# Kernel optimization log

Hardware: AMD Instinct MI355X
Metric: run time of the kernel (lower is better)

The kernel has to match this reference:

```python
import jax, jax.numpy as jnp
import numpy as np

N_HEAD = 16
D_HEAD = 64


def setup_inputs() -> dict:
    key = jax.random.key(0)
    k1, k2, k3, k4 = jax.random.split(key, 4)
    T, B, D = 1024, 8, 1024
    input = jax.random.normal(k1, (T, B, D), dtype=jnp.float32)
    pos_enc = jax.random.normal(k2, (T, B, D), dtype=jnp.float32) * 0.1
    # causal mask: True = masked (future positions), broadcast over batch
    causal = jnp.triu(jnp.ones((T, T), dtype=bool), k=1)
    attn_mask = jnp.broadcast_to(causal[None, :, :], (B, T, T))
    W_qkv = jax.random.normal(k3, (D, 3 * N_HEAD * D_HEAD), dtype=jnp.float32) * (D ** -0.5)
    W_o = jax.random.normal(k4, (N_HEAD * D_HEAD, N_HEAD * D_HEAD), dtype=jnp.float32) * ((N_HEAD * D_HEAD) ** -0.5)
    return {"input": input, "pos_enc": pos_enc, "attn_mask": attn_mask,
            "W_qkv": W_qkv, "W_o": W_o}


def reference(input, pos_enc, attn_mask, W_qkv, W_o):
    T, B, D = input.shape
    scale = 1.0 / (D_HEAD ** 0.5)
    # attn_type == 2: qkv on (w + r)
    heads = (input + pos_enc) @ W_qkv                      # [T,B,3*n*d]
    q, k, v = jnp.split(heads, 3, axis=-1)
    q = q.reshape(T, B, N_HEAD, D_HEAD)
    k = k.reshape(T, B, N_HEAD, D_HEAD)
    v = v.reshape(T, B, N_HEAD, D_HEAD)
    # scores [B, n, qlen, klen]
    score = jnp.einsum('ibnd,jbnd->bnij', q, k) * scale
    score = jnp.where(attn_mask[:, None, :, :], -jnp.inf, score)
    prob = jax.nn.softmax(score.astype(jnp.float32), axis=-1)  # [B,n,i,j]
    # coverage: mean over heads -> [B,i,j], then transpose -> [B,j,i]
    coverage = jnp.mean(prob, axis=1).transpose(0, 2, 1)
    # dropout is identity at eval (dropatt=0)
    attn_vec = jnp.einsum('bnij,jbnd->ibnd', prob, v)       # [T,B,n,d]
    attn_vec = attn_vec.reshape(T, B, N_HEAD * D_HEAD)
    attn_out = attn_vec @ W_o
    return attn_out, coverage
```

## Files before the change

kernel.cpp:

```cpp
#include <hip/hip_runtime.h>
#include <hip/hip_bf16.h>


typedef __bf16 v8bf __attribute__((ext_vector_type(8)));
typedef float  v4f  __attribute__((ext_vector_type(4)));
typedef unsigned short v8us __attribute__((ext_vector_type(8)));

#define MFMA16x16x32(a, b, c) __builtin_amdgcn_mfma_f32_16x16x32_bf16(a, b, c, 0, 0, 0)

#define GLD_LDS16(g, l) \
    __builtin_amdgcn_global_load_lds((const __attribute__((address_space(1))) void*)(g), \
                                     (__attribute__((address_space(3))) void*)(l), 16, 0, 0)

__device__ __forceinline__ unsigned short f2bf(float f) {
    unsigned int u = __float_as_uint(f);
    u = (u + 0x7FFF + ((u >> 16) & 1)) >> 16;
    return (unsigned short)u;
}

__global__ __launch_bounds__(256) void prep_x(const float* __restrict__ in,
                                              const float* __restrict__ pe,
                                              unsigned short* __restrict__ x) {
    size_t idx = ((size_t)blockIdx.x * 256 + threadIdx.x) * 8;
    v4f a0 = *(const v4f*)(in + idx);
    v4f a1 = *(const v4f*)(in + idx + 4);
    v4f p0 = *(const v4f*)(pe + idx);
    v4f p1 = *(const v4f*)(pe + idx + 4);
    v8us r;
    unsigned short* rp = (unsigned short*)&r;
#pragma unroll
    for (int q = 0; q < 4; q++) {
        rp[q]     = f2bf(a0[q] + p0[q]);
        rp[q + 4] = f2bf(a1[q] + p1[q]);
    }
    *(v8us*)(x + idx) = r;
}

__global__ __launch_bounds__(256) void transpose_f32_bf16(const float* __restrict__ src,
                                                          unsigned short* __restrict__ dst,
                                                          int R, int C) {
    __shared__ alignas(16) unsigned short t[64][72];
    int c0 = blockIdx.x * 64, r0 = blockIdx.y * 64;
    int tid = threadIdx.x;
    int rr = tid >> 2, cg = (tid & 3) * 16;
    const float* s = src + (size_t)(r0 + rr) * C + c0 + cg;
#pragma unroll
    for (int q4 = 0; q4 < 4; q4++) {
        v4f v = *(const v4f*)(s + q4 * 4);
#pragma unroll
        for (int q = 0; q < 4; q++) t[rr][cg + q4 * 4 + q] = f2bf(v[q]);
    }
    __syncthreads();
    v8us o0, o1;
    unsigned short* o0p = (unsigned short*)&o0;
    unsigned short* o1p = (unsigned short*)&o1;
#pragma unroll
    for (int q = 0; q < 8; q++) {
        o0p[q] = t[cg + q][rr];
        o1p[q] = t[cg + 8 + q][rr];
    }
    *(v8us*)(dst + (size_t)(c0 + rr) * R + r0 + cg)     = o0;
    *(v8us*)(dst + (size_t)(c0 + rr) * R + r0 + cg + 8) = o1;
}

__global__ __launch_bounds__(256) void transpose_v(const unsigned short* __restrict__ heads,
                                                   unsigned short* __restrict__ Vt) {
    __shared__ alignas(16) unsigned short t[64][72];
    const int bn = blockIdx.y, b = bn >> 4, n = bn & 15;
    const int j0 = blockIdx.x * 64;
    const int tid = threadIdx.x;
    const int jr = tid >> 2, dg = (tid & 3) * 16;
    const unsigned short* s = heads + ((size_t)(j0 + jr) * 8 + b) * 3072 + 2048 + n * 64 + dg;
    *(v8us*)&t[jr][dg]     = *(const v8us*)(s);
    *(v8us*)&t[jr][dg + 8] = *(const v8us*)(s + 8);
    __syncthreads();
    const int dr = tid >> 2, jg = (tid & 3) * 16;
    v8us o0, o1;
    unsigned short* o0p = (unsigned short*)&o0;
    unsigned short* o1p = (unsigned short*)&o1;
#pragma unroll
    for (int q = 0; q < 8; q++) {
        o0p[q] = t[jg + q][dr];
        o1p[q] = t[jg + 8 + q][dr];
    }
    unsigned short* d = Vt + ((size_t)bn * 64 + dr) * 1024 + j0 + jg;
    *(v8us*)(d)     = o0;
    *(v8us*)(d + 8) = o1;
}

template <bool F32OUT>
__global__ __launch_bounds__(256) void gemm_bf16_v2(const unsigned short* __restrict__ A,
                                                    const unsigned short* __restrict__ Bt,
                                                    void* __restrict__ Cout,
                                                    int M, int N, int K) {
    __shared__ alignas(16) unsigned short As[128 * 64];
    __shared__ alignas(16) unsigned short Bs[128 * 64];

    const int nwgx = gridDim.x;
    const int id   = blockIdx.y * nwgx + blockIdx.x;
    const int cpx  = (nwgx * gridDim.y) >> 3;
    const int id2  = (id & 7) * cpx + (id >> 3);
    const int m0 = (id2 / nwgx) * 128, n0 = (id2 % nwgx) * 128;

    const int tid = threadIdx.x;
    const int lane = tid & 63, wave = tid >> 6;
    const int quad = lane >> 4, lq = lane & 15, lq7 = lq & 7;
    const int mW = (wave & 1) * 64, nW = (wave >> 1) * 64;

    v4f acc[4][4];
#pragma unroll
    for (int mi = 0; mi < 4; mi++)
#pragma unroll
        for (int ni = 0; ni < 4; ni++) acc[mi][ni] = (v4f){0.f, 0.f, 0.f, 0.f};

    const int lr = lane >> 3, lu = lane & 7;
    const int ug = lu ^ lr;
    const unsigned short* agl = A  + (size_t)(m0 + wave * 32 + lr) * K + ug * 8;
    const unsigned short* bgl = Bt + (size_t)(n0 + wave * 32 + lr) * K + ug * 8;
    unsigned short* AsW = (unsigned short*)As + wave * 32 * 64;
    unsigned short* BsW = (unsigned short*)Bs + wave * 32 * 64;

    for (int k0 = 0; k0 < K; k0 += 64) {
        __syncthreads();
#pragma unroll
        for (int t = 0; t < 4; t++) {
            GLD_LDS16(agl + k0 + (size_t)t * 8 * K, AsW + t * 512);
            GLD_LDS16(bgl + k0 + (size_t)t * 8 * K, BsW + t * 512);
        }
        __syncthreads();
#pragma unroll
        for (int h = 0; h < 2; h++) {
            v8bf af[4], bfr[4];
#pragma unroll
            for (int mi = 0; mi < 4; mi++)
                af[mi] = *(const v8bf*)&As[(mW + mi * 16 + lq) * 64 + (((quad + 4 * h) ^ lq7) * 8)];
#pragma unroll
            for (int ni = 0; ni < 4; ni++)
                bfr[ni] = *(const v8bf*)&Bs[(nW + ni * 16 + lq) * 64 + (((quad + 4 * h) ^ lq7) * 8)];
#pragma unroll
            for (int mi = 0; mi < 4; mi++)
#pragma unroll
                for (int ni = 0; ni < 4; ni++)
                    acc[mi][ni] = MFMA16x16x32(af[mi], bfr[ni], acc[mi][ni]);
        }
    }

#pragma unroll
    for (int mi = 0; mi < 4; mi++)
#pragma unroll
        for (int ni = 0; ni < 4; ni++)
#pragma unroll
            for (int r = 0; r < 4; r++) {
                int row = m0 + mW + mi * 16 + quad * 4 + r;
                int col = n0 + nW + ni * 16 + lq;
                if (F32OUT)
                    ((float*)Cout)[(size_t)row * N + col] = acc[mi][ni][r];
                else
                    ((unsigned short*)Cout)[(size_t)row * N + col] = f2bf(acc[mi][ni][r]);
            }
}

#define AT_T  1024
#define AT_B  8
#define AT_NH 16
#define AT_HS 3072
#define AT_ALPHA 0.18033688011112042f

__global__ __launch_bounds__(256) void attn_fused5(const unsigned short* __restrict__ heads,
                                                   const unsigned short* __restrict__ Vt,
                                                   unsigned short* __restrict__ av,
                                                   float* __restrict__ lBuf) {
    __shared__ alignas(16) unsigned short KL[64 * 64];
    __shared__ alignas(16) unsigned short VL[64 * 64];
    __shared__ alignas(16) unsigned short Ps[4 * 16 * 32];
    const int bn = blockIdx.x, b = bn >> 4, n = bn & 15;
    const int y = blockIdx.y;
    const int g = (y < 8) ? (15 - y) : (y - 8);
    const int tid = threadIdx.x;
    const int wv = tid >> 6, lane = tid & 63;
    const int quad = lane >> 4, lq = lane & 15;
    const int i0 = g * 64 + wv * 16;
    const int imax = i0 + 15;

    size_t qbase = ((size_t)(i0 + lq) * 8 + b) * AT_HS + n * 64 + quad * 8;
    v8bf q0 = *(const v8bf*)(heads + qbase);
    v8bf q1 = *(const v8bf*)(heads + qbase + 32);

    const int srow = tid >> 3, sunit = tid & 7;
    const size_t kRowStride = (size_t)8 * AT_HS;
    const unsigned short* kg = heads + ((size_t)srow * 8 + b) * AT_HS + 1024 + n * 64 + sunit * 8;
    const unsigned short* vg = Vt + ((size_t)bn * 64 + srow) * 1024 + sunit * 8;
    const int swz = ((sunit ^ (srow & 7)) * 8);
    unsigned short* kw0 = KL + srow * 64 + swz;
    unsigned short* kw1 = KL + (srow + 32) * 64 + swz;
    unsigned short* vw0 = VL + srow * 64 + swz;
    unsigned short* vw1 = VL + (srow + 32) * 64 + swz;

    v8us kr0 = *(const v8us*)(kg);
    v8us kr1 = *(const v8us*)(kg + 32 * kRowStride);
    v8us vr0 = *(const v8us*)(vg);
    v8us vr1 = *(const v8us*)(vg + 32 * 1024);

    unsigned short* psw = Ps + wv * 512;
    const v8bf* pr = (const v8bf*)(psw + lq * 32 + ((quad ^ (lq & 3)) * 8));
    const int lq7 = lq & 7, lqh = lq >> 3;

    float Sl[4] = {0.f, 0.f, 0.f, 0.f};
    v4f o[4];
#pragma unroll
    for (int dt = 0; dt < 4; dt++) o[dt] = (v4f){0.f, 0.f, 0.f, 0.f};

    for (int c = 0; c <= g; ++c) {
        __syncthreads();
        *(v8us*)kw0 = kr0; *(v8us*)kw1 = kr1;
        *(v8us*)vw0 = vr0; *(v8us*)vw1 = vr1;
        __syncthreads();
        if (c < g) {
            const unsigned short* kgn = kg + (size_t)(c + 1) * 64 * kRowStride;
            kr0 = *(const v8us*)(kgn);
            kr1 = *(const v8us*)(kgn + 32 * kRowStride);
            const unsigned short* vgn = vg + (c + 1) * 64;
            vr0 = *(const v8us*)(vgn);
            vr1 = *(const v8us*)(vgn + 32 * 1024);
        }
        const int jb = c * 64;
#pragma unroll
        for (int jj = 0; jj < 64; jj += 32) {
            const int j0 = jb + jj;
            if (j0 <= imax) {
                const v8bf ka = *(const v8bf*)(KL + (jj + lq) * 64      + ((quad ^ lq7) * 8));
                const v8bf kb = *(const v8bf*)(KL + (jj + lq) * 64      + (((4 + quad) ^ lq7) * 8));
                const v8bf kc = *(const v8bf*)(KL + (jj + 16 + lq) * 64 + ((quad ^ lq7) * 8));
                const v8bf kd = *(const v8bf*)(KL + (jj + 16 + lq) * 64 + (((4 + quad) ^ lq7) * 8));
                v4f s0 = (v4f){0.f, 0.f, 0.f, 0.f}, s1 = s0;
                s0 = MFMA16x16x32(q0, ka, s0);
                s0 = MFMA16x16x32(q1, kb, s0);
                s1 = MFMA16x16x32(q0, kc, s1);
                s1 = MFMA16x16x32(q1, kd, s1);
                const int ja = j0 + lq, jb2 = j0 + 16 + lq;
#pragma unroll
                for (int r = 0; r < 4; ++r) {
                    const int i = i0 + quad * 4 + r;
                    float e0 = exp2f(s0[r] * AT_ALPHA);
                    float e1 = exp2f(s1[r] * AT_ALPHA);
                    float p0 = (ja  <= i) ? e0 : 0.f;
                    float p1 = (jb2 <= i) ? e1 : 0.f;
                    Sl[r] += p0 + p1;
                    psw[(quad * 4 + r) * 32 + ((lqh ^ r) * 8) + lq7]        = f2bf(p0);
                    psw[(quad * 4 + r) * 32 + (((lqh | 2) ^ r) * 8) + lq7]  = f2bf(p1);
                }
                const v8bf pf = *pr;
#pragma unroll
                for (int dt = 0; dt < 4; ++dt) {
                    const v8bf vf = *(const v8bf*)(VL + (dt * 16 + lq) * 64 +
                                                   ((((jj >> 3) + quad) ^ lq7) * 8));
                    o[dt] = MFMA16x16x32(pf, vf, o[dt]);
                }
            }
        }
    }

#pragma unroll
    for (int mask = 1; mask < 16; mask <<= 1)
#pragma unroll
        for (int r = 0; r < 4; r++)
            Sl[r] += __shfl_xor(Sl[r], mask);
    float linv[4];
#pragma unroll
    for (int r = 0; r < 4; r++) linv[r] = __builtin_amdgcn_rcpf(Sl[r]);
    if (lq == 0) {
#pragma unroll
        for (int r = 0; r < 4; r++) {
            int i = i0 + quad * 4 + r;
            lBuf[(size_t)bn * AT_T + i] = Sl[r];
        }
    }
#pragma unroll
    for (int dt = 0; dt < 4; dt++)
#pragma unroll
        for (int r = 0; r < 4; r++) {
            int i = i0 + quad * 4 + r;
            av[((size_t)i * 8 + b) * 1024 + n * 64 + dt * 16 + lq] = f2bf(o[dt][r] * linv[r]);
        }
}

__global__ __launch_bounds__(256) void coverage3(const unsigned short* __restrict__ heads,
                                                 const float* __restrict__ lBuf,
                                                 float* __restrict__ cov) {
    const int jt64 = blockIdx.x, it64 = blockIdx.y, b = blockIdx.z;
    const int i0 = it64 * 64, j0 = jt64 * 64;
    const int tid = threadIdx.x;

    if (jt64 > it64) {
        float* base = cov + (size_t)b * 1048576 + (size_t)(j0 + (tid >> 2)) * 1024
                      + i0 + (tid & 3) * 16;
        v4f z = (v4f){0.f, 0.f, 0.f, 0.f};
#pragma unroll
        for (int q = 0; q < 4; q++) *(v4f*)(base + q * 4) = z;
        return;
    }

    __shared__ alignas(16) char smem[64 * 68 * 4];
    unsigned short* QL = (unsigned short*)smem;
    unsigned short* KL = (unsigned short*)(smem + 8192);
    float* TF = (float*)smem;

    const int wv = tid >> 6, lane = tid & 63;
    const int quad = lane >> 4, lq = lane & 15, lq7 = lq & 7;
    const bool diag = (it64 == jt64);
    const int jtmax = diag ? wv : 3;

    const int srow = tid >> 3, sunit = tid & 7;
    const unsigned short* qgb = heads + ((size_t)(i0 + srow) * 8 + b) * AT_HS + sunit * 8;
    const unsigned short* kgb = heads + ((size_t)(j0 + srow) * 8 + b) * AT_HS + 1024 + sunit * 8;
    const int rowOff32 = 32 * 8 * AT_HS;
    const int swz = (sunit ^ (srow & 7)) * 8;
    unsigned short* qw0 = QL + srow * 64 + swz;
    unsigned short* qw1 = QL + (srow + 32) * 64 + swz;
    unsigned short* kw0 = KL + srow * 64 + swz;
    unsigned short* kw1 = KL + (srow + 32) * 64 + swz;

    v8us qr0 = *(const v8us*)(qgb);
    v8us qr1 = *(const v8us*)(qgb + rowOff32);
    v8us kr0 = *(const v8us*)(kgb);
    v8us kr1 = *(const v8us*)(kgb + rowOff32);

    v4f acc[4];
#pragma unroll
    for (int jt = 0; jt < 4; jt++) acc[jt] = (v4f){0.f, 0.f, 0.f, 0.f};

    const float* lrow = lBuf + (size_t)b * 16 * AT_T + i0 + wv * 16 + quad * 4;

    for (int n = 0; n < 16; ++n) {
        __syncthreads();
        *(v8us*)qw0 = qr0; *(v8us*)qw1 = qr1;
        *(v8us*)kw0 = kr0; *(v8us*)kw1 = kr1;
        __syncthreads();
        if (n < 15) {
            qr0 = *(const v8us*)(qgb + (n + 1) * 64);
            qr1 = *(const v8us*)(qgb + (n + 1) * 64 + rowOff32);
            kr0 = *(const v8us*)(kgb + (n + 1) * 64);
            kr1 = *(const v8us*)(kgb + (n + 1) * 64 + rowOff32);
        }
        v4f lv = *(const v4f*)(lrow + (size_t)n * AT_T);
        float linv[4];
#pragma unroll
        for (int r = 0; r < 4; r++) linv[r] = __builtin_amdgcn_rcpf(lv[r]);

        const v8bf qa = *(const v8bf*)(QL + (wv * 16 + lq) * 64 + ((quad ^ lq7) * 8));
        const v8bf qb = *(const v8bf*)(QL + (wv * 16 + lq) * 64 + (((4 + quad) ^ lq7) * 8));
#pragma unroll
        for (int jt = 0; jt < 4; jt++) {
            if (jt <= jtmax) {
                const v8bf ka = *(const v8bf*)(KL + (jt * 16 + lq) * 64 + ((quad ^ lq7) * 8));
                const v8bf kb = *(const v8bf*)(KL + (jt * 16 + lq) * 64 + (((4 + quad) ^ lq7) * 8));
                v4f s = (v4f){0.f, 0.f, 0.f, 0.f};
                s = MFMA16x16x32(qa, ka, s);
                s = MFMA16x16x32(qb, kb, s);
#pragma unroll
                for (int r = 0; r < 4; r++) {
                    float e = exp2f(s[r] * AT_ALPHA);
                    if (diag && jt == wv && lq > quad * 4 + r) e = 0.f;
                    acc[jt][r] = fmaf(e, linv[r], acc[jt][r]);
                }
            }
        }
    }

    __syncthreads();
#pragma unroll
    for (int jt = 0; jt < 4; jt++) {
        v4f w = acc[jt] * 0.0625f;
        *(v4f*)(TF + (size_t)(jt * 16 + lq) * 68 + wv * 16 + quad * 4) = w;
    }
    __syncthreads();
    {
        const int jl = tid >> 2, cg = (tid & 3) * 16;
        float* dst = cov + (size_t)b * 1048576 + (size_t)(j0 + jl) * 1024 + i0 + cg;
        const float* src = TF + (size_t)jl * 68 + cg;
#pragma unroll
        for (int q = 0; q < 4; q++) *(v4f*)(dst + q * 4) = *(const v4f*)(src + q * 4);
    }
}

extern "C" void kernel_launch(void* const* d_in, const int* in_sizes, int n_in,
                              void* d_out, int out_size, void* d_ws, size_t ws_size,
                              hipStream_t stream) {
    const float* input = (const float*)d_in[0];
    const float* pos   = (const float*)d_in[1];
    const float* Wqkv  = (const float*)d_in[3];
    const float* Wo    = (const float*)d_in[4];
    float* out = (float*)d_out;

    char* ws = (char*)d_ws;
    if (ws_size < 93323264) return;
    unsigned short* x     = (unsigned short*)(ws);
    unsigned short* heads = (unsigned short*)(ws + 16777216);
    unsigned short* av    = (unsigned short*)(ws + 67108864);
    unsigned short* WqkvT = (unsigned short*)(ws + 83886080);
    unsigned short* WoT   = (unsigned short*)(ws + 90177536);
    float* lBuf = (float*)(ws + 92798976);
    unsigned short* Vt = x;

    prep_x<<<4096, 256, 0, stream>>>(input, pos, x);
    transpose_f32_bf16<<<dim3(48, 16), 256, 0, stream>>>(Wqkv, WqkvT, 1024, 3072);
    transpose_f32_bf16<<<dim3(16, 16), 256, 0, stream>>>(Wo, WoT, 1024, 1024);
    gemm_bf16_v2<false><<<dim3(24, 64), 256, 0, stream>>>(x, WqkvT, heads, 8192, 3072, 1024);
    transpose_v<<<dim3(16, 128), 256, 0, stream>>>(heads, Vt);
    attn_fused5<<<dim3(128, 16), 256, 0, stream>>>(heads, Vt, av, lBuf);
    coverage3<<<dim3(16, 16, 8), 256, 0, stream>>>(heads, lBuf, out + 8388608);
    gemm_bf16_v2<true><<<dim3(8, 64), 256, 0, stream>>>(av, WoT, out, 8192, 1024, 1024);
}
```

Measured before the change: 337.8 us.

## Fuse prep kernels and double-buffer K with direct Q loads in coverage

Merges the input-add and the two weight-transpose kernels into one launch, which removes two kernel launches. The coverage kernel now reads Q fragments straight from global memory into registers instead of staging them through LDS. K tiles are double-buffered in LDS, cutting the per-head barriers from two to one. The row-tile order is also reversed so the heavier lower-triangle blocks get scheduled first. The risk is less coalesced Q reads from global memory.

New measurement: 361.1 us. 1.07x slower.

```diff
diff --git a/kernel.cpp b/kernel.cpp
--- a/kernel.cpp
+++ b/kernel.cpp
@@ -18,30 +18,11 @@
     return (unsigned short)u;
 }
 
-__global__ __launch_bounds__(256) void prep_x(const float* __restrict__ in,
-                                              const float* __restrict__ pe,
-                                              unsigned short* __restrict__ x) {
-    size_t idx = ((size_t)blockIdx.x * 256 + threadIdx.x) * 8;
-    v4f a0 = *(const v4f*)(in + idx);
-    v4f a1 = *(const v4f*)(in + idx + 4);
-    v4f p0 = *(const v4f*)(pe + idx);
-    v4f p1 = *(const v4f*)(pe + idx + 4);
-    v8us r;
-    unsigned short* rp = (unsigned short*)&r;
-#pragma unroll
-    for (int q = 0; q < 4; q++) {
-        rp[q]     = f2bf(a0[q] + p0[q]);
-        rp[q + 4] = f2bf(a1[q] + p1[q]);
-    }
-    *(v8us*)(x + idx) = r;
-}
-
-__global__ __launch_bounds__(256) void transpose_f32_bf16(const float* __restrict__ src,
-                                                          unsigned short* __restrict__ dst,
-                                                          int R, int C) {
-    __shared__ alignas(16) unsigned short t[64][72];
-    int c0 = blockIdx.x * 64, r0 = blockIdx.y * 64;
-    int tid = threadIdx.x;
+__device__ __forceinline__ void transpose_tile_f32_bf16(const float* __restrict__ src,
+                                                        unsigned short* __restrict__ dst,
+                                                        int R, int C, int bx, int by,
+                                                        int tid, unsigned short (*t)[72]) {
+    int c0 = bx * 64, r0 = by * 64;
     int rr = tid >> 2, cg = (tid & 3) * 16;
     const float* s = src + (size_t)(r0 + rr) * C + c0 + cg;
 #pragma unroll
@@ -61,6 +42,38 @@
     }
     *(v8us*)(dst + (size_t)(c0 + rr) * R + r0 + cg)     = o0;
     *(v8us*)(dst + (size_t)(c0 + rr) * R + r0 + cg + 8) = o1;
+}
+
+__global__ __launch_bounds__(256) void prep_all(const float* __restrict__ in,
+                                                const float* __restrict__ pe,
+                                                unsigned short* __restrict__ x,
+                                                const float* __restrict__ Wqkv,
+                                                unsigned short* __restrict__ WqkvT,
+                                                const float* __restrict__ Wo,
+                                                unsigned short* __restrict__ WoT) {
+    __shared__ alignas(16) unsigned short t[64][72];
+    const int id = blockIdx.x, tid = threadIdx.x;
+    if (id < 4096) {
+        size_t idx = ((size_t)id * 256 + tid) * 8;
+        v4f a0 = *(const v4f*)(in + idx);
+        v4f a1 = *(const v4f*)(in + idx + 4);
+        v4f p0 = *(const v4f*)(pe + idx);
+        v4f p1 = *(const v4f*)(pe + idx + 4);
+        v8us r;
+        unsigned short* rp = (unsigned short*)&r;
+#pragma unroll
+        for (int q = 0; q < 4; q++) {
+            rp[q]     = f2bf(a0[q] + p0[q]);
+            rp[q + 4] = f2bf(a1[q] + p1[q]);
+        }
+        *(v8us*)(x + idx) = r;
+    } else if (id < 4864) {
+        int r = id - 4096;
+        transpose_tile_f32_bf16(Wqkv, WqkvT, 1024, 3072, r % 48, r / 48, tid, t);
+    } else {
+        int r = id - 4864;
+        transpose_tile_f32_bf16(Wo, WoT, 1024, 1024, r % 16, r / 16, tid, t);
+    }
 }
 
 __global__ __launch_bounds__(256) void transpose_v(const unsigned short* __restrict__ heads,
@@ -284,10 +297,10 @@
         }
 }
 
-__global__ __launch_bounds__(256) void coverage3(const unsigned short* __restrict__ heads,
+__global__ __launch_bounds__(256) void coverage4(const unsigned short* __restrict__ heads,
                                                  const float* __restrict__ lBuf,
                                                  float* __restrict__ cov) {
-    const int jt64 = blockIdx.x, it64 = blockIdx.y, b = blockIdx.z;
+    const int jt64 = blockIdx.x, it64 = 15 - blockIdx.y, b = blockIdx.z;
     const int i0 = it64 * 64, j0 = jt64 * 64;
     const int tid = threadIdx.x;
 
@@ -300,9 +313,9 @@
         return;
     }
 
-    __shared__ alignas(16) char smem[64 * 68 * 4];
-    unsigned short* QL = (unsigned short*)smem;
-    unsigned short* KL = (unsigned short*)(smem + 8192);
+    __shared__ alignas(16) char smem[17408];
+    unsigned short* KL0 = (unsigned short*)smem;
+    unsigned short* KL1 = (unsigned short*)(smem + 8192);
     float* TF = (float*)smem;
 
     const int wv = tid >> 6, lane = tid & 63;
@@ -311,19 +324,13 @@
     const int jtmax = diag ? wv : 3;
 
     const int srow = tid >> 3, sunit = tid & 7;
-    const unsigned short* qgb = heads + ((size_t)(i0 + srow) * 8 + b) * AT_HS + sunit * 8;
     const unsigned short* kgb = heads + ((size_t)(j0 + srow) * 8 + b) * AT_HS + 1024 + sunit * 8;
     const int rowOff32 = 32 * 8 * AT_HS;
     const int swz = (sunit ^ (srow & 7)) * 8;
-    unsigned short* qw0 = QL + srow * 64 + swz;
-    unsigned short* qw1 = QL + (srow + 32) * 64 + swz;
-    unsigned short* kw0 = KL + srow * 64 + swz;
-    unsigned short* kw1 = KL + (srow + 32) * 64 + swz;
-
-    v8us qr0 = *(const v8us*)(qgb);
-    v8us qr1 = *(const v8us*)(qgb + rowOff32);
-    v8us kr0 = *(const v8us*)(kgb);
-    v8us kr1 = *(const v8us*)(kgb + rowOff32);
+    const int kwo0 = srow * 64 + swz;
+    const int kwo1 = (srow + 32) * 64 + swz;
+
+    const unsigned short* qrow = heads + ((size_t)(i0 + wv * 16 + lq) * 8 + b) * AT_HS + quad * 8;
 
     v4f acc[4];
 #pragma unroll
@@ -331,32 +338,36 @@
 
     const float* lrow = lBuf + (size_t)b * 16 * AT_T + i0 + wv * 16 + quad * 4;
 
-    for (int n = 0; n < 16; ++n) {
-        __syncthreads();
-        *(v8us*)qw0 = qr0; *(v8us*)qw1 = qr1;
-        *(v8us*)kw0 = kr0; *(v8us*)kw1 = kr1;
-        __syncthreads();
-        if (n < 15) {
-            qr0 = *(const v8us*)(qgb + (n + 1) * 64);
-            qr1 = *(const v8us*)(qgb + (n + 1) * 64 + rowOff32);
+    {
+        v8us k0 = *(const v8us*)(kgb);
+        v8us k1 = *(const v8us*)(kgb + rowOff32);
+        *(v8us*)(KL0 + kwo0) = k0;
+        *(v8us*)(KL0 + kwo1) = k1;
+    }
+    __syncthreads();
+
+    auto covHead = [&](int n, unsigned short* KLc, unsigned short* KLn) {
+        v8us kr0, kr1;
+        const bool pf = (n < 15);
+        if (pf) {
             kr0 = *(const v8us*)(kgb + (n + 1) * 64);
             kr1 = *(const v8us*)(kgb + (n + 1) * 64 + rowOff32);
         }
+        v8bf q0 = *(const v8bf*)(qrow + n * 64);
+        v8bf q1 = *(const v8bf*)(qrow + n * 64 + 32);
         v4f lv = *(const v4f*)(lrow + (size_t)n * AT_T);
         float linv[4];
 #pragma unroll
         for (int r = 0; r < 4; r++) linv[r] = __builtin_amdgcn_rcpf(lv[r]);
 
-        const v8bf qa = *(const v8bf*)(QL + (wv * 16 + lq) * 64 + ((quad ^ lq7) * 8));
-        const v8bf qb = *(const v8bf*)(QL + (wv * 16 + lq) * 64 + (((4 + quad) ^ lq7) * 8));
 #pragma unroll
         for (int jt = 0; jt < 4; jt++) {
             if (jt <= jtmax) {
-                const v8bf ka = *(const v8bf*)(KL + (jt * 16 + lq) * 64 + ((quad ^ lq7) * 8));
-                const v8bf kb = *(const v8bf*)(KL + (jt * 16 + lq) * 64 + (((4 + quad) ^ lq7) * 8));
+                const v8bf ka = *(const v8bf*)(KLc + (jt * 16 + lq) * 64 + ((quad ^ lq7) * 8));
+                const v8bf kb = *(const v8bf*)(KLc + (jt * 16 + lq) * 64 + (((4 + quad) ^ lq7) * 8));
                 v4f s = (v4f){0.f, 0.f, 0.f, 0.f};
-                s = MFMA16x16x32(qa, ka, s);
-                s = MFMA16x16x32(qb, kb, s);
+                s = MFMA16x16x32(q0, ka, s);
+                s = MFMA16x16x32(q1, kb, s);
 #pragma unroll
                 for (int r = 0; r < 4; r++) {
                     float e = exp2f(s[r] * AT_ALPHA);
@@ -365,6 +376,16 @@
                 }
             }
         }
+        if (pf) {
+            *(v8us*)(KLn + kwo0) = kr0;
+            *(v8us*)(KLn + kwo1) = kr1;
+            __syncthreads();
+        }
+    };
+
+    for (int n = 0; n < 16; n += 2) {
+        covHead(n,     KL0, KL1);
+        covHead(n + 1, KL1, KL0);
     }
 
     __syncthreads();
@@ -402,12 +423,10 @@
     float* lBuf = (float*)(ws + 92798976);
     unsigned short* Vt = x;
 
-    prep_x<<<4096, 256, 0, stream>>>(input, pos, x);
-    transpose_f32_bf16<<<dim3(48, 16), 256, 0, stream>>>(Wqkv, WqkvT, 1024, 3072);
-    transpose_f32_bf16<<<dim3(16, 16), 256, 0, stream>>>(Wo, WoT, 1024, 1024);
+    prep_all<<<5120, 256, 0, stream>>>(input, pos, x, Wqkv, WqkvT, Wo, WoT);
     gemm_bf16_v2<false><<<dim3(24, 64), 256, 0, stream>>>(x, WqkvT, heads, 8192, 3072, 1024);
     transpose_v<<<dim3(16, 128), 256, 0, stream>>>(heads, Vt);
     attn_fused5<<<dim3(128, 16), 256, 0, stream>>>(heads, Vt, av, lBuf);
-    coverage3<<<dim3(16, 16, 8), 256, 0, stream>>>(heads, lBuf, out + 8388608);
+    coverage4<<<dim3(16, 16, 8), 256, 0, stream>>>(heads, lBuf, out + 8388608);
     gemm_bf16_v2<true><<<dim3(8, 64), 256, 0, stream>>>(av, WoT, out, 8192, 1024, 1024);
 }
```
